# Performance work log

Measured on AMD Instinct MI355X. Metric: run time of the kernel, lower is better.

The kernel has to match this reference:

```python
import jax, jax.numpy as jnp
import numpy as np

TAU = 2.0
EPS_COH = 1e-8
EPS_NLL = 1e-7
ALPHA = 0.0
# component-vs-modality mask: rows = (common, synergy, g_spec, p_spec), cols = (gene, path)
MASK = np.array([[1.0, 1.0], [0.0, 0.0], [1.0, 0.0], [0.0, 1.0]], dtype=np.float32)


def l2norm(x, axis=-1):
    n = jnp.sqrt(jnp.sum(x * x, axis=axis, keepdims=True))
    return x / jnp.maximum(n, 1e-12)


def setup_inputs() -> dict:
    key = jax.random.key(0)
    ks = jax.random.split(key, 8)
    B, K, C, N = 64, 4, 256, 8192
    hazards = jax.random.uniform(ks[0], (B, K), dtype=jnp.float32)
    S = jnp.cumprod(1.0 - hazards, axis=1)  # survival curve, matches torch semantics
    indiv = jax.random.normal(ks[1], (B, 4, C), dtype=jnp.float32)
    gene = jax.random.normal(ks[2], (B, 1, C), dtype=jnp.float32)
    path = jax.random.normal(ks[3], (B, 1, C), dtype=jnp.float32)
    cohort_bank = jax.random.normal(ks[4], (K, N, 4, C), dtype=jnp.float32)
    label = jax.random.randint(ks[5], (B,), 0, K).astype(jnp.int32)
    c = jax.random.randint(ks[6], (B,), 0, 2).astype(jnp.int32)
    return {"hazards": hazards, "S": S, "indiv": indiv, "gene": gene,
            "path": path, "cohort_bank": cohort_bank, "label": label, "c": c}


def reference(hazards, S, indiv, gene, path, cohort_bank, label, c):
    B, K = hazards.shape
    dt = hazards.dtype
    # ---- NLLSurvLoss ----
    cf = c.astype(dt)[:, None]                       # [B,1] censoring flag
    Y = label.astype(jnp.int32)[:, None]             # [B,1]
    S_padded = jnp.concatenate([jnp.ones((B, 1), dt), S], axis=1)  # [B,K+1]
    s_y = jnp.take_along_axis(S_padded, Y, axis=1)
    h_y = jnp.take_along_axis(hazards, Y, axis=1)
    s_y1 = jnp.take_along_axis(S_padded, Y + 1, axis=1)
    clamp = lambda x: jnp.maximum(x, EPS_NLL)
    uncensored = -(1.0 - cf) * (jnp.log(clamp(s_y)) + jnp.log(clamp(h_y)))
    censored = -cf * jnp.log(clamp(s_y1))
    neg_l = censored + uncensored
    nll = ((1.0 - ALPHA) * neg_l + ALPHA * uncensored).mean()
    # ---- CohortLoss: intra ----
    indiv_n = l2norm(indiv)                          # [B,4,C]
    gp_n = l2norm(jnp.concatenate([gene, path], axis=1))  # [B,2,C]
    sim = jnp.einsum('bpc,btc->bpt', indiv_n, gp_n)  # [B,4,2]
    mask = jnp.asarray(MASK, dtype=dt)               # [4,2]
    intra = (jnp.abs(sim) * (1.0 - mask) - mask * sim).mean(axis=(1, 2)) + 1.0
    intra_loss = intra.mean()
    # ---- CohortLoss: inter (vectorized cohort-bank retrieval) ----
    n_cls, N = cohort_bank.shape[0], cohort_bank.shape[1]
    anchors = l2norm(indiv.mean(axis=1))             # [B,C]
    bank_means = cohort_bank.mean(axis=2)            # [n_cls,N,C]
    bank_n = l2norm(bank_means)                      # [n_cls,N,C]
    sims = jnp.einsum('knc,bc->bkn', bank_n, anchors)  # [B,n_cls,N]
    e = jnp.exp(sims / TAU)
    pos_mask = (label[:, None] == jnp.arange(n_cls, dtype=label.dtype)[None, :]).astype(dt)[:, :, None]  # [B,n_cls,1]
    ep = jnp.sum(e * pos_mask) / (B * N)                       # mean over B*N positive sims
    en = jnp.sum(e * (1.0 - pos_mask)) / (B * (n_cls - 1) * N)  # mean over B*(n_cls-1)*N negative sims
    inter_loss = -jnp.log((ep + EPS_COH) / (ep + en + EPS_COH))
    cohort_loss = intra_loss + inter_loss
    # Loss_factory: total = 1.0*nllsurv + 1.0*cohort
    return nll + cohort_loss
```

## Files before the change

kernel.cpp:

```cpp
#include <hip/hip_runtime.h>
#include <math.h>

#define BB 64
#define KK 4
#define CC 256
#define NN 8192
#define NROWS (KK*NN)
#define GRID_F 512
#define WPG 4

#define WS_B_OFF     0
#define WS_SLOT_OFF  32768
#define WS_NLL_OFF   40960
#define WS_INTRA_OFF 41216
#define WS_TKT_OFF   41472

#define EPS_NLL 1e-7f

typedef __attribute__((ext_vector_type(8))) short bf16x8;
typedef __attribute__((ext_vector_type(4))) float f32x4;

__device__ __forceinline__ float4 f4add(float4 a, float4 b){ return make_float4(a.x+b.x, a.y+b.y, a.z+b.z, a.w+b.w); }
__device__ __forceinline__ float4 f4scale(float4 a, float s){ return make_float4(a.x*s, a.y*s, a.z*s, a.w*s); }
__device__ __forceinline__ float dot4(float4 a, float4 b){ return a.x*b.x + a.y*b.y + a.z*b.z + a.w*b.w; }

__device__ __forceinline__ float wred(float v){
#pragma unroll
  for (int m = 32; m >= 1; m >>= 1) v += __shfl_xor(v, m, 64);
  return v;
}

__device__ __forceinline__ unsigned short f2bf(float x){
  union { float f; unsigned u; } v; v.f = x;
  unsigned r = v.u + 0x7fffu + ((v.u >> 16) & 1u);
  return (unsigned short)(r >> 16);
}

__global__ __launch_bounds__(64) void prep_kernel(
    const float* __restrict__ hazards, const float* __restrict__ S,
    const float* __restrict__ indiv,   const float* __restrict__ gene,
    const float* __restrict__ path,    const int* __restrict__ label,
    const int* __restrict__ cvec,      char* __restrict__ ws)
{
  const int b = blockIdx.x;
  const int lane = threadIdx.x;

  const float4* ind4 = (const float4*)indiv + (size_t)b * 256;
  float4 i0 = ind4[  0 + lane];
  float4 i1 = ind4[ 64 + lane];
  float4 i2 = ind4[128 + lane];
  float4 i3 = ind4[192 + lane];
  float4 g  = ((const float4*)gene)[b*64 + lane];
  float4 p  = ((const float4*)path)[b*64 + lane];

  float4 am = f4scale(f4add(f4add(i0, i1), f4add(i2, i3)), 0.25f);
  float na = sqrtf(wred(dot4(am, am)));
  float4 an = f4scale(am, 1.0f / fmaxf(na, 1e-12f));

  {
    const int cq = lane;
    const unsigned addr = (unsigned)((cq >> 3) * 4096
                        + (b >> 4) * 1024
                        + ((((cq >> 1) & 3) * 16) + (b & 15)) * 16
                        + (cq & 1) * 8);
    ushort4 h4;
    h4.x = f2bf(an.x); h4.y = f2bf(an.y); h4.z = f2bf(an.z); h4.w = f2bf(an.w);
    *(ushort4*)(ws + WS_B_OFF + addr) = h4;
  }

  float4 v[6] = {i0, i1, i2, i3, g, p};
#pragma unroll
  for (int j = 0; j < 6; ++j) {
    float n = sqrtf(wred(dot4(v[j], v[j])));
    v[j] = f4scale(v[j], 1.0f / fmaxf(n, 1e-12f));
  }

  float s[4][2];
#pragma unroll
  for (int pp = 0; pp < 4; ++pp)
#pragma unroll
    for (int t = 0; t < 2; ++t)
      s[pp][t] = wred(dot4(v[pp], v[4+t]));

  if (lane == 0) {
    float intra = (-s[0][0]) + (-s[0][1])
                + fabsf(s[1][0]) + fabsf(s[1][1])
                + (-s[2][0]) + fabsf(s[2][1])
                + fabsf(s[3][0]) + (-s[3][1]);
    intra = intra * 0.125f + 1.0f;
    ((float*)(ws + WS_INTRA_OFF))[b] = intra;

    int   Y  = label[b];
    float cf = (float)cvec[b];
    float s_y  = (Y == 0) ? 1.0f : S[b*KK + Y - 1];
    float s_y1 = S[b*KK + Y];
    float h_y  = hazards[b*KK + Y];
    float neg_l = -cf * logf(fmaxf(s_y1, EPS_NLL))
                  - (1.0f - cf) * (logf(fmaxf(s_y, EPS_NLL)) + logf(fmaxf(h_y, EPS_NLL)));
    ((float*)(ws + WS_NLL_OFF))[b] = neg_l;
  }
}

__global__ __launch_bounds__(256, 2) void fused_kernel(
    const float* __restrict__ bank, const int* __restrict__ label,
    char* __restrict__ ws, float* __restrict__ out)
{
  __shared__ uint4 Bl[2048];
  __shared__ uint4 At4[WPG][512];
  __shared__ double redw[WPG][2];
  __shared__ unsigned tkt_s;

  const int tid  = threadIdx.x;
  const int wave = tid >> 6;
  const int lane = tid & 63;
  const int lm   = lane & 15;
  const int lg   = lane >> 4;

  const uint4* Bg = (const uint4*)(ws + WS_B_OFF);
#pragma unroll
  for (int i = 0; i < 8; ++i) Bl[tid + i*256] = Bg[tid + i*256];
  __syncthreads();

  const int gw   = blockIdx.x * WPG + wave;
  const int row0 = gw * 16;
  const int kk   = row0 >> 13;
  char* At = (char*)&At4[wave][0];

  int lab[4];
#pragma unroll
  for (int nt = 0; nt < 4; ++nt) lab[nt] = label[nt*16 + lm];

  const float4* b4 = (const float4*)bank;

#pragma unroll 1
  for (int pass = 0; pass < 4; ++pass) {
    const int rp0 = row0 + pass * 4;

    float4 r[4][4];
#pragma unroll
    for (int rr = 0; rr < 4; ++rr)
#pragma unroll
      for (int c = 0; c < 4; ++c)
        r[rr][c] = b4[(size_t)(rp0 + rr) * 256 + c * 64 + lane];

#pragma unroll
    for (int rr = 0; rr < 4; ++rr) {
      float4 m = f4add(f4add(r[rr][0], r[rr][1]), f4add(r[rr][2], r[rr][3]));
      float ss = wred(dot4(m, m));
      float rs = rsqrtf(fmaxf(ss, 1e-24f));
      const int lr = pass * 4 + rr;
      ushort4 h4;
      h4.x = f2bf(m.x * rs); h4.y = f2bf(m.y * rs);
      h4.z = f2bf(m.z * rs); h4.w = f2bf(m.w * rs);
      *(ushort4*)(At + lr*512 + ((lane*8) ^ ((lr & 7) << 4))) = h4;
    }
  }

  bf16x8 af[8];
#pragma unroll
  for (int kc = 0; kc < 8; ++kc)
    af[kc] = *(const bf16x8*)(At + lm*512 + ((kc*64 + lg*16) ^ ((lm & 7) << 4)));

  f32x4 acc0 = {0,0,0,0}, acc1 = {0,0,0,0}, acc2 = {0,0,0,0}, acc3 = {0,0,0,0};
#pragma unroll
  for (int kc = 0; kc < 8; ++kc) {
    acc0 = __builtin_amdgcn_mfma_f32_16x16x32_bf16(af[kc], *(const bf16x8*)&Bl[(kc*4+0)*64 + lane], acc0, 0, 0, 0);
    acc1 = __builtin_amdgcn_mfma_f32_16x16x32_bf16(af[kc], *(const bf16x8*)&Bl[(kc*4+1)*64 + lane], acc1, 0, 0, 0);
    acc2 = __builtin_amdgcn_mfma_f32_16x16x32_bf16(af[kc], *(const bf16x8*)&Bl[(kc*4+2)*64 + lane], acc2, 0, 0, 0);
    acc3 = __builtin_amdgcn_mfma_f32_16x16x32_bf16(af[kc], *(const bf16x8*)&Bl[(kc*4+3)*64 + lane], acc3, 0, 0, 0);
  }

  float epf = 0.0f, enf = 0.0f;
#define DO_NT(ACC, NT)                                                        \
  {                                                                           \
    float es = expf(ACC.x * 0.5f) + expf(ACC.y * 0.5f)                        \
             + expf(ACC.z * 0.5f) + expf(ACC.w * 0.5f);                       \
    if (lab[NT] == kk) epf += es; else enf += es;                             \
  }
  DO_NT(acc0, 0) DO_NT(acc1, 1) DO_NT(acc2, 2) DO_NT(acc3, 3)
#undef DO_NT

  epf = wred(epf);
  enf = wred(enf);
  if (lane == 0) {
    redw[wave][0] = (double)epf;
    redw[wave][1] = (double)enf;
  }
  __syncthreads();

  double*   slots  = (double*)(ws + WS_SLOT_OFF);
  unsigned* ticket = (unsigned*)(ws + WS_TKT_OFF);

  if (tid == 0) {
    double bep = 0.0, ben = 0.0;
#pragma unroll
    for (int w = 0; w < WPG; ++w) { bep += redw[w][0]; ben += redw[w][1]; }
    slots[blockIdx.x*2 + 0] = bep;
    slots[blockIdx.x*2 + 1] = ben;
    __threadfence();
    tkt_s = atomicAdd(ticket, 1u);
  }
  __syncthreads();

  if (tkt_s == GRID_F - 1 && wave == 0) {
    __threadfence();
    double pep = 0.0, pen = 0.0;
    for (int i = lane; i < GRID_F; i += 64) {
      pep += slots[2*i + 0];
      pen += slots[2*i + 1];
    }
#pragma unroll
    for (int m = 32; m >= 1; m >>= 1) {
      pep += __shfl_xor(pep, m, 64);
      pen += __shfl_xor(pen, m, 64);
    }
    float scal = ((const float*)(ws + WS_NLL_OFF))[lane]
               + ((const float*)(ws + WS_INTRA_OFF))[lane];
    scal = wred(scal);
    if (lane == 0) {
      double ep = pep / (double)(BB * NN);
      double en = pen / (double)(BB * (KK-1) * NN);
      double inter = -log((ep + 1e-8) / (ep + en + 1e-8));
      out[0] = (float)((double)scal / 64.0 + inter);
    }
  }
}

extern "C" void kernel_launch(void* const* d_in, const int* in_sizes, int n_in,
                              void* d_out, int out_size, void* d_ws, size_t ws_size,
                              hipStream_t stream)
{
  const float* hazards = (const float*)d_in[0];
  const float* S       = (const float*)d_in[1];
  const float* indiv   = (const float*)d_in[2];
  const float* gene    = (const float*)d_in[3];
  const float* path    = (const float*)d_in[4];
  const float* bank    = (const float*)d_in[5];
  const int*   label   = (const int*)d_in[6];
  const int*   cvec    = (const int*)d_in[7];
  char*  ws  = (char*)d_ws;
  float* out = (float*)d_out;

  hipMemsetAsync(ws + WS_TKT_OFF, 0, 4, stream);
  prep_kernel<<<dim3(BB), dim3(64), 0, stream>>>(hazards, S, indiv, gene, path, label, cvec, ws);
  fused_kernel<<<dim3(GRID_F), dim3(256), 0, stream>>>(bank, label, ws, out);
}
```

Measured before the change: 234.5 us.

## Split each row tile across two waves and read B fragments directly from global

Doubles waves per block so each 16-row bank tile is loaded and normalized by two waves (8 rows each), with register double-buffering of the bank loads. The shared-memory copy of the anchor matrix is removed, and MFMA B fragments are read straight from the workspace with prefetch, each wave computing half of the output columns. The aim is more memory-level parallelism on the dominant streaming read of the bank, plus removal of the per-block LDS staging. In exchange it adds a block-wide barrier and redundant global/L2 reads of B.

```diff
diff --git a/kernel.cpp b/kernel.cpp
--- a/kernel.cpp
+++ b/kernel.cpp
@@ -7,7 +7,7 @@
 #define NN 8192
 #define NROWS (KK*NN)
 #define GRID_F 512
-#define WPG 4
+#define WPG 8
 
 #define WS_B_OFF     0
 #define WS_SLOT_OFF  32768
@@ -101,12 +101,11 @@
   }
 }
 
-__global__ __launch_bounds__(256, 2) void fused_kernel(
+__global__ __launch_bounds__(512, 4) void fused_kernel(
     const float* __restrict__ bank, const int* __restrict__ label,
     char* __restrict__ ws, float* __restrict__ out)
 {
-  __shared__ uint4 Bl[2048];
-  __shared__ uint4 At4[WPG][512];
+  __shared__ uint4 At4[WPG/2][512];
   __shared__ double redw[WPG][2];
   __shared__ unsigned tkt_s;
 
@@ -116,39 +115,41 @@
   const int lm   = lane & 15;
   const int lg   = lane >> 4;
 
-  const uint4* Bg = (const uint4*)(ws + WS_B_OFF);
-#pragma unroll
-  for (int i = 0; i < 8; ++i) Bl[tid + i*256] = Bg[tid + i*256];
-  __syncthreads();
-
-  const int gw   = blockIdx.x * WPG + wave;
-  const int row0 = gw * 16;
-  const int kk   = row0 >> 13;
-  char* At = (char*)&At4[wave][0];
-
-  int lab[4];
-#pragma unroll
-  for (int nt = 0; nt < 4; ++nt) lab[nt] = label[nt*16 + lm];
+  const int tileInWG = wave >> 1;
+  const int sub      = wave & 1;
+  const int gtile    = blockIdx.x * (WPG/2) + tileInWG;
+  const int row0     = gtile * 16;
+  const int kk       = row0 >> 13;
+  char* At = (char*)&At4[tileInWG][0];
 
   const float4* b4 = (const float4*)bank;
-
-#pragma unroll 1
-  for (int pass = 0; pass < 4; ++pass) {
-    const int rp0 = row0 + pass * 4;
-
-    float4 r[4][4];
-#pragma unroll
-    for (int rr = 0; rr < 4; ++rr)
-#pragma unroll
-      for (int c = 0; c < 4; ++c)
-        r[rr][c] = b4[(size_t)(rp0 + rr) * 256 + c * 64 + lane];
-
-#pragma unroll
-    for (int rr = 0; rr < 4; ++rr) {
-      float4 m = f4add(f4add(r[rr][0], r[rr][1]), f4add(r[rr][2], r[rr][3]));
+  const int rbase = row0 + sub * 8;
+
+  float4 rbuf[2][2][4];
+#pragma unroll
+  for (int rr = 0; rr < 2; ++rr)
+#pragma unroll
+    for (int c = 0; c < 4; ++c)
+      rbuf[0][rr][c] = b4[(size_t)(rbase + rr) * 256 + c * 64 + lane];
+
+#pragma unroll
+  for (int p = 0; p < 4; ++p) {
+    const int cur = p & 1;
+    if (p < 3) {
+      const int nxt = cur ^ 1;
+#pragma unroll
+      for (int rr = 0; rr < 2; ++rr)
+#pragma unroll
+        for (int c = 0; c < 4; ++c)
+          rbuf[nxt][rr][c] = b4[(size_t)(rbase + (p+1)*2 + rr) * 256 + c * 64 + lane];
+    }
+#pragma unroll
+    for (int rr = 0; rr < 2; ++rr) {
+      float4 m = f4add(f4add(rbuf[cur][rr][0], rbuf[cur][rr][1]),
+                       f4add(rbuf[cur][rr][2], rbuf[cur][rr][3]));
       float ss = wred(dot4(m, m));
       float rs = rsqrtf(fmaxf(ss, 1e-24f));
-      const int lr = pass * 4 + rr;
+      const int lr = sub * 8 + p * 2 + rr;
       ushort4 h4;
       h4.x = f2bf(m.x * rs); h4.y = f2bf(m.y * rs);
       h4.z = f2bf(m.z * rs); h4.w = f2bf(m.w * rs);
@@ -156,29 +157,46 @@
     }
   }
 
+  __syncthreads();
+
   bf16x8 af[8];
 #pragma unroll
   for (int kc = 0; kc < 8; ++kc)
     af[kc] = *(const bf16x8*)(At + lm*512 + ((kc*64 + lg*16) ^ ((lm & 7) << 4)));
 
-  f32x4 acc0 = {0,0,0,0}, acc1 = {0,0,0,0}, acc2 = {0,0,0,0}, acc3 = {0,0,0,0};
+  const char* Bg = ws + WS_B_OFF;
+  const int nt0 = sub * 2;
+  int lab0 = label[nt0*16 + lm];
+  int lab1 = label[(nt0+1)*16 + lm];
+
+  f32x4 acc0 = {0,0,0,0}, acc1 = {0,0,0,0};
+  bf16x8 bfr[2][2];
+#pragma unroll
+  for (int nt = 0; nt < 2; ++nt)
+    bfr[0][nt] = *(const bf16x8*)(Bg + (0*4 + nt0 + nt)*1024 + lane*16);
+
 #pragma unroll
   for (int kc = 0; kc < 8; ++kc) {
-    acc0 = __builtin_amdgcn_mfma_f32_16x16x32_bf16(af[kc], *(const bf16x8*)&Bl[(kc*4+0)*64 + lane], acc0, 0, 0, 0);
-    acc1 = __builtin_amdgcn_mfma_f32_16x16x32_bf16(af[kc], *(const bf16x8*)&Bl[(kc*4+1)*64 + lane], acc1, 0, 0, 0);
-    acc2 = __builtin_amdgcn_mfma_f32_16x16x32_bf16(af[kc], *(const bf16x8*)&Bl[(kc*4+2)*64 + lane], acc2, 0, 0, 0);
-    acc3 = __builtin_amdgcn_mfma_f32_16x16x32_bf16(af[kc], *(const bf16x8*)&Bl[(kc*4+3)*64 + lane], acc3, 0, 0, 0);
+    const int cur = kc & 1;
+    if (kc < 7) {
+      const int nxt = cur ^ 1;
+#pragma unroll
+      for (int nt = 0; nt < 2; ++nt)
+        bfr[nxt][nt] = *(const bf16x8*)(Bg + ((kc+1)*4 + nt0 + nt)*1024 + lane*16);
+    }
+    acc0 = __builtin_amdgcn_mfma_f32_16x16x32_bf16(af[kc], bfr[cur][0], acc0, 0, 0, 0);
+    acc1 = __builtin_amdgcn_mfma_f32_16x16x32_bf16(af[kc], bfr[cur][1], acc1, 0, 0, 0);
   }
 
   float epf = 0.0f, enf = 0.0f;
-#define DO_NT(ACC, NT)                                                        \
-  {                                                                           \
-    float es = expf(ACC.x * 0.5f) + expf(ACC.y * 0.5f)                        \
-             + expf(ACC.z * 0.5f) + expf(ACC.w * 0.5f);                       \
-    if (lab[NT] == kk) epf += es; else enf += es;                             \
-  }
-  DO_NT(acc0, 0) DO_NT(acc1, 1) DO_NT(acc2, 2) DO_NT(acc3, 3)
-#undef DO_NT
+  {
+    float es0 = expf(acc0.x * 0.5f) + expf(acc0.y * 0.5f)
+              + expf(acc0.z * 0.5f) + expf(acc0.w * 0.5f);
+    if (lab0 == kk) epf += es0; else enf += es0;
+    float es1 = expf(acc1.x * 0.5f) + expf(acc1.y * 0.5f)
+              + expf(acc1.z * 0.5f) + expf(acc1.w * 0.5f);
+    if (lab1 == kk) epf += es1; else enf += es1;
+  }
 
   epf = wred(epf);
   enf = wred(enf);
@@ -243,5 +261,5 @@
 
   hipMemsetAsync(ws + WS_TKT_OFF, 0, 4, stream);
   prep_kernel<<<dim3(BB), dim3(64), 0, stream>>>(hazards, S, indiv, gene, path, label, cvec, ws);
-  fused_kernel<<<dim3(GRID_F), dim3(256), 0, stream>>>(bank, label, ws, out);
-}
+  fused_kernel<<<dim3(GRID_F), dim3(512), 0, stream>>>(bank, label, ws, out);
+}
```

New measurement: 229.4 us. 2.2% less time.
